# Kernel tuning notes

Measured on AMD Instinct MI355X. Metric: run time of the kernel, lower is better.

## Reference

```python
import jax, jax.numpy as jnp
import numpy as np

N, E, D, H = 50000, 800000, 128, 4
EPS = 1e-5


def setup_inputs() -> dict:
    key = jax.random.key(0)
    ks = jax.random.split(key, 12)
    s_in = 1.0 / np.sqrt(D)
    s_att = 1.0 / np.sqrt(D)
    inp = {
        "x": jax.random.normal(ks[0], (N, D), dtype=jnp.float32),
        "edge_index": jax.random.randint(ks[1], (2, E), 0, N, dtype=jnp.int32),
        # conv1 params: W [D, H*D], att_src/att_dst [H, D], bias [D]
        "W1": jax.random.normal(ks[2], (D, H * D), dtype=jnp.float32) * s_in,
        "as1": jax.random.normal(ks[3], (H, D), dtype=jnp.float32) * s_att,
        "ad1": jax.random.normal(ks[4], (H, D), dtype=jnp.float32) * s_att,
        "b1": jnp.zeros((D,), dtype=jnp.float32),
        "g1": jnp.ones((D,), dtype=jnp.float32),
        "be1": jnp.zeros((D,), dtype=jnp.float32),
        # conv2 params
        "W2": jax.random.normal(ks[5], (D, H * D), dtype=jnp.float32) * s_in,
        "as2": jax.random.normal(ks[6], (H, D), dtype=jnp.float32) * s_att,
        "ad2": jax.random.normal(ks[7], (H, D), dtype=jnp.float32) * s_att,
        "b2": jnp.zeros((D,), dtype=jnp.float32),
        "g2": jnp.ones((D,), dtype=jnp.float32),
        "be2": jnp.zeros((D,), dtype=jnp.float32),
    }
    return inp


def _gat_conv(x, src, dst, W, att_src, att_dst, bias):
    # project: [N, H, C]
    h = (x @ W).reshape(N, H, D)
    a_src = jnp.einsum("nhc,hc->nh", h, att_src)  # [N, H]
    a_dst = jnp.einsum("nhc,hc->nh", h, att_dst)  # [N, H]
    # attention logits per edge, softmax over incoming edges of each dst
    logits = jax.nn.leaky_relu(a_src[src] + a_dst[dst], negative_slope=0.2)  # [Etot, H]
    lmax = jax.ops.segment_max(logits, dst, num_segments=N)  # [N, H]
    p = jnp.exp(logits - lmax[dst])
    denom = jax.ops.segment_sum(p, dst, num_segments=N)  # [N, H]
    alpha = p / denom[dst]  # self-loops guarantee denom > 0
    # weighted scatter-add aggregation
    msg = h[src] * alpha[:, :, None]  # [Etot, H, C]
    out = jax.ops.segment_sum(msg, dst, num_segments=N)  # [N, H, C]
    return out.mean(axis=1) + bias  # concat=False: mean over heads


def _batchnorm_relu(x, gamma, beta):
    mu = x.mean(axis=0)
    var = x.var(axis=0)  # biased, as torch uses for normalization
    xn = (x - mu) * jax.lax.rsqrt(var + EPS)
    return jax.nn.relu(xn * gamma + beta)


def reference(x, edge_index, W1, as1, ad1, b1, g1, be1, W2, as2, ad2, b2, g2, be2):
    # add self loops (GATConv default add_self_loops=True)
    loop = jnp.arange(N, dtype=edge_index.dtype)
    src = jnp.concatenate([edge_index[0], loop])
    dst = jnp.concatenate([edge_index[1], loop])
    x = _batchnorm_relu(_gat_conv(x, src, dst, W1, as1, ad1, b1), g1, be1)
    x = _batchnorm_relu(_gat_conv(x, src, dst, W2, as2, ad2, b2), g2, be2)
    return x
```

## Files before the change

### kernel.cpp

```cpp
#include <hip/hip_runtime.h>
#include <hip/hip_bf16.h>
#include <hip/hip_fp16.h>
#include <math.h>

#define NN 50000
#define NP 50048
#define NE 800000
#define ET (NE + NN)
#define DF 128
#define NH 4
#define HD 512
#define BN_EPS 1e-5f

typedef __hip_bfloat16 bf16;
typedef __attribute__((ext_vector_type(8))) short bf16x8;
typedef __attribute__((ext_vector_type(4))) float f32x4;

__global__ __launch_bounds__(256) void cvt_x_bf16(const float* __restrict__ in, bf16* __restrict__ out) {
    int i = blockIdx.x * 256 + threadIdx.x;
    if (i >= NN * DF / 4) return;
    float4 v = reinterpret_cast<const float4*>(in)[i];
    union { bf16 b[4]; short4 s; } u;
    u.b[0] = __float2bfloat16(v.x); u.b[1] = __float2bfloat16(v.y);
    u.b[2] = __float2bfloat16(v.z); u.b[3] = __float2bfloat16(v.w);
    reinterpret_cast<short4*>(out)[i] = u.s;
}

__global__ __launch_bounds__(256) void make_wsd(const float* __restrict__ W1, const float* __restrict__ as1,
                                                const float* __restrict__ ad1,
                                                const float* __restrict__ W2, const float* __restrict__ as2,
                                                const float* __restrict__ ad2,
                                                float* __restrict__ wsd) {
    int t = blockIdx.x * 256 + threadIdx.x;
    if (t >= 2048) return;
    int layer = t >> 10;
    int o = (t >> 7) & 7;
    int d = t & 127;
    int h = o & 3;
    const float* W  = layer ? W2 : W1;
    const float* av = layer ? (o < 4 ? as2 : ad2) : (o < 4 ? as1 : ad1);
    const float* wrow = W + d * HD + h * DF;
    const float* arow = av + h * DF;
    float sum = 0.f;
    for (int c = 0; c < DF; ++c) sum += wrow[c] * arow[c];
    wsd[layer * 1024 + o * DF + d] = sum;
}

__global__ __launch_bounds__(256) void cvt_bt2(const float* __restrict__ W1, const float* __restrict__ W2,
                                               bf16* __restrict__ B1, bf16* __restrict__ B2) {
    int i = blockIdx.x * 256 + threadIdx.x;
    if (i >= 2 * DF * HD) return;
    int layer = i >> 16;
    int ii = i & 65535;
    int c = ii >> 9, k = ii & 511;
    int h = k >> 7, d = k & 127;
    const float* W = layer ? W2 : W1;
    bf16* B = layer ? B2 : B1;
    B[ii] = __float2bfloat16(0.25f * W[d * HD + h * DF + c]);
}

__global__ __launch_bounds__(256) void xscore(const bf16* __restrict__ X,
                                              const float* __restrict__ wsd,
                                              float* __restrict__ a_src,
                                              float* __restrict__ a_dst) {
    __shared__ float w[8][DF];
    reinterpret_cast<float4*>(&w[0][0])[threadIdx.x] = reinterpret_cast<const float4*>(wsd)[threadIdx.x];
    __syncthreads();
    const int n = blockIdx.x * 4 + (threadIdx.x >> 6);
    const int l = threadIdx.x & 63;
    unsigned xv = reinterpret_cast<const unsigned*>(X)[n * 64 + l];
    float x0 = __uint_as_float(xv << 16);
    float x1 = __uint_as_float(xv & 0xffff0000u);
    float v[8];
    #pragma unroll
    for (int o = 0; o < 8; ++o)
        v[o] = x0 * w[o][2 * l] + x1 * w[o][2 * l + 1];
    #pragma unroll
    for (int off = 1; off < 64; off <<= 1) {
        #pragma unroll
        for (int o = 0; o < 8; ++o) v[o] += __shfl_xor(v[o], off);
    }
    if (l == 0) {
        reinterpret_cast<float4*>(a_src)[n] = make_float4(v[0], v[1], v[2], v[3]);
        reinterpret_cast<float4*>(a_dst)[n] = make_float4(v[4], v[5], v[6], v[7]);
    }
}

__global__ __launch_bounds__(256) void count_rank(const int* __restrict__ ei, int* __restrict__ counts,
                                                  int* __restrict__ rank) {
    int e = (blockIdx.x * 256 + threadIdx.x) * 2;
    if (e >= ET) return;
    int d0, d1;
    if (e + 1 < NE) {
        int2 dd = *reinterpret_cast<const int2*>(ei + NE + e);
        d0 = dd.x; d1 = dd.y;
    } else {
        d0 = (e < NE) ? ei[NE + e] : (e - NE);
        d1 = (e + 1 < NE) ? ei[NE + e + 1] : (e + 1 - NE);
    }
    rank[e]     = atomicAdd(&counts[d0 << 4], 1);
    rank[e + 1] = atomicAdd(&counts[d1 << 4], 1);
}

__global__ __launch_bounds__(256) void scan1(const int* __restrict__ counts, int* __restrict__ bsum) {
    __shared__ int sd[256];
    int i = blockIdx.x * 256 + threadIdx.x;
    sd[threadIdx.x] = (i < NN) ? counts[i << 4] : 0;
    __syncthreads();
    for (int s = 128; s > 0; s >>= 1) {
        if (threadIdx.x < s) sd[threadIdx.x] += sd[threadIdx.x + s];
        __syncthreads();
    }
    if (threadIdx.x == 0) bsum[blockIdx.x] = sd[0];
}

__global__ __launch_bounds__(256) void scan2(int* __restrict__ bsum, int nb) {
    __shared__ int sd[256];
    int i = threadIdx.x;
    int v = (i < nb) ? bsum[i] : 0;
    sd[i] = v;
    __syncthreads();
    for (int s = 1; s < 256; s <<= 1) {
        int t = sd[i];
        int u = (i >= s) ? sd[i - s] : 0;
        __syncthreads();
        sd[i] = t + u;
        __syncthreads();
    }
    if (i < nb) bsum[i] = sd[i] - v;
}

__global__ __launch_bounds__(256) void scan3(const int* __restrict__ counts, const int* __restrict__ bsum,
                                             int* __restrict__ row_ptr) {
    __shared__ int sd[256];
    int i = blockIdx.x * 256 + threadIdx.x;
    int v = (i < NN) ? counts[i << 4] : 0;
    sd[threadIdx.x] = v;
    __syncthreads();
    for (int s = 1; s < 256; s <<= 1) {
        int t = sd[threadIdx.x];
        int u = (threadIdx.x >= s) ? sd[threadIdx.x - s] : 0;
        __syncthreads();
        sd[threadIdx.x] = t + u;
        __syncthreads();
    }
    int excl = sd[threadIdx.x] - v + bsum[blockIdx.x];
    if (i < NN) row_ptr[i] = excl;
    if (i == 0) row_ptr[NN] = ET;
}

__global__ __launch_bounds__(256) void fill_scatter(const int* __restrict__ ei, const int* __restrict__ rank,
                                                    const int* __restrict__ row_ptr, int* __restrict__ col) {
    int e = (blockIdx.x * 256 + threadIdx.x) * 2;
    if (e >= ET) return;
    int s0, d0, s1, d1;
    if (e + 1 < NE) {
        int2 ss = *reinterpret_cast<const int2*>(ei + e);
        int2 dd = *reinterpret_cast<const int2*>(ei + NE + e);
        s0 = ss.x; s1 = ss.y; d0 = dd.x; d1 = dd.y;
    } else {
        if (e < NE) { s0 = ei[e]; d0 = ei[NE + e]; } else { s0 = d0 = e - NE; }
        if (e + 1 < NE) { s1 = ei[e + 1]; d1 = ei[NE + e + 1]; } else { s1 = d1 = e + 1 - NE; }
    }
    int2 rk = *reinterpret_cast<const int2*>(rank + e);
    col[row_ptr[d0] + rk.x] = s0;
    col[row_ptr[d1] + rk.y] = s1;
}

__global__ __launch_bounds__(256) void edge_alpha(const float* __restrict__ a_src,
                                                  const float* __restrict__ a_dst,
                                                  const int* __restrict__ row_ptr,
                                                  const int* __restrict__ col,
                                                  uint4* __restrict__ rec) {
    const int n = blockIdx.x * 4 + (threadIdx.x >> 6);
    const int l = threadIdx.x & 63;
    const int start = row_ptr[n], end = row_ptr[n + 1];
    const float4 ad4 = reinterpret_cast<const float4*>(a_dst)[n];
    const float4* __restrict__ as4 = reinterpret_cast<const float4*>(a_src);
    if (end - start <= 64) {
        const int j = start + l;
        int cj = 0;
        float lv[4] = {-1e30f, -1e30f, -1e30f, -1e30f};
        if (j < end) {
            cj = col[j];
            float4 a = as4[cj];
            lv[0] = a.x + ad4.x; lv[1] = a.y + ad4.y; lv[2] = a.z + ad4.z; lv[3] = a.w + ad4.w;
            #pragma unroll
            for (int h = 0; h < 4; ++h) lv[h] = lv[h] > 0.f ? lv[h] : 0.2f * lv[h];
        }
        float m[4], p[4], s[4];
        #pragma unroll
        for (int h = 0; h < 4; ++h) m[h] = lv[h];
        #pragma unroll
        for (int off = 1; off < 64; off <<= 1) {
            #pragma unroll
            for (int h = 0; h < 4; ++h) m[h] = fmaxf(m[h], __shfl_xor(m[h], off));
        }
        #pragma unroll
        for (int h = 0; h < 4; ++h) { p[h] = (j < end) ? __expf(lv[h] - m[h]) : 0.f; s[h] = p[h]; }
        #pragma unroll
        for (int off = 1; off < 64; off <<= 1) {
            #pragma unroll
            for (int h = 0; h < 4; ++h) s[h] += __shfl_xor(s[h], off);
        }
        if (j < end) {
            __half2 a01 = __floats2half2_rn(p[0] / s[0], p[1] / s[1]);
            __half2 a23 = __floats2half2_rn(p[2] / s[2], p[3] / s[3]);
            uint4 r;
            r.x = *reinterpret_cast<unsigned*>(&a01);
            r.y = *reinterpret_cast<unsigned*>(&a23);
            r.z = (unsigned)cj;
            r.w = 0;
            rec[j] = r;
        }
    } else {
        float m[4] = {-1e30f, -1e30f, -1e30f, -1e30f}, s[4] = {0.f, 0.f, 0.f, 0.f};
        for (int base = start; base < end; base += 64) {
            const int j = base + l;
            float lv[4] = {-1e30f, -1e30f, -1e30f, -1e30f};
            if (j < end) {
                float4 a = as4[col[j]];
                lv[0] = a.x + ad4.x; lv[1] = a.y + ad4.y; lv[2] = a.z + ad4.z; lv[3] = a.w + ad4.w;
                #pragma unroll
                for (int h = 0; h < 4; ++h) lv[h] = lv[h] > 0.f ? lv[h] : 0.2f * lv[h];
            }
            float cm[4], cp[4];
            #pragma unroll
            for (int h = 0; h < 4; ++h) cm[h] = lv[h];
            #pragma unroll
            for (int off = 1; off < 64; off <<= 1) {
                #pragma unroll
                for (int h = 0; h < 4; ++h) cm[h] = fmaxf(cm[h], __shfl_xor(cm[h], off));
            }
            #pragma unroll
            for (int h = 0; h < 4; ++h) {
                float nm = fmaxf(m[h], cm[h]);
                cp[h] = (j < end) ? __expf(lv[h] - nm) : 0.f;
                s[h] *= __expf(m[h] - nm);
                m[h] = nm;
            }
            #pragma unroll
            for (int off = 1; off < 64; off <<= 1) {
                #pragma unroll
                for (int h = 0; h < 4; ++h) cp[h] += __shfl_xor(cp[h], off);
            }
            #pragma unroll
            for (int h = 0; h < 4; ++h) s[h] += cp[h];
        }
        for (int base = start; base < end; base += 64) {
            const int j = base + l;
            if (j < end) {
                int cj = col[j];
                float4 a = as4[cj];
                float v0 = a.x + ad4.x, v1 = a.y + ad4.y, v2 = a.z + ad4.z, v3 = a.w + ad4.w;
                v0 = v0 > 0.f ? v0 : 0.2f * v0; v1 = v1 > 0.f ? v1 : 0.2f * v1;
                v2 = v2 > 0.f ? v2 : 0.2f * v2; v3 = v3 > 0.f ? v3 : 0.2f * v3;
                __half2 a01 = __floats2half2_rn(__expf(v0 - m[0]) / s[0], __expf(v1 - m[1]) / s[1]);
                __half2 a23 = __floats2half2_rn(__expf(v2 - m[2]) / s[2], __expf(v3 - m[3]) / s[3]);
                uint4 r;
                r.x = *reinterpret_cast<unsigned*>(&a01);
                r.y = *reinterpret_cast<unsigned*>(&a23);
                r.z = (unsigned)cj;
                r.w = 0;
                rec[j] = r;
            }
        }
    }
}

#define EDGE(xu, r) {                                                                \
    float lo = __uint_as_float((xu) << 16);                                          \
    float hi = __uint_as_float((xu) & 0xffff0000u);                                  \
    float2 f01 = __half22float2(*reinterpret_cast<const __half2*>(&(r).x));          \
    float2 f23 = __half22float2(*reinterpret_cast<const __half2*>(&(r).y));          \
    acc[0][0] += f01.x * lo; acc[0][1] += f01.x * hi;                                \
    acc[1][0] += f01.y * lo; acc[1][1] += f01.y * hi;                                \
    acc[2][0] += f23.x * lo; acc[2][1] += f23.x * hi;                                \
    acc[3][0] += f23.y * lo; acc[3][1] += f23.y * hi; }

__global__ __launch_bounds__(256) void aggregate_x(const bf16* __restrict__ X,
                                                   const uint4* __restrict__ rec,
                                                   const int* __restrict__ row_ptr,
                                                   bf16* __restrict__ aggX) {
    const int n = blockIdx.x * 4 + (threadIdx.x >> 6);
    const int l = threadIdx.x & 63;
    const int start = row_ptr[n], end = row_ptr[n + 1];
    const unsigned* __restrict__ X4 = reinterpret_cast<const unsigned*>(X);
    float acc[4][2] = {};
    int j = start;
    for (; j + 4 <= end; j += 4) {
        uint4 r0 = rec[j], r1 = rec[j + 1], r2 = rec[j + 2], r3 = rec[j + 3];
        unsigned x0 = X4[(size_t)r0.z * 64 + l];
        unsigned x1 = X4[(size_t)r1.z * 64 + l];
        unsigned x2 = X4[(size_t)r2.z * 64 + l];
        unsigned x3 = X4[(size_t)r3.z * 64 + l];
        EDGE(x0, r0) EDGE(x1, r1) EDGE(x2, r2) EDGE(x3, r3)
    }
    for (; j < end; ++j) {
        uint4 r0 = rec[j];
        unsigned x0 = X4[(size_t)r0.z * 64 + l];
        EDGE(x0, r0)
    }
    unsigned* outp = reinterpret_cast<unsigned*>(aggX) + (size_t)n * 256;
    #pragma unroll
    for (int h = 0; h < 4; ++h) {
        union { bf16 b; unsigned short u; } plo, phi;
        plo.b = __float2bfloat16(acc[h][0]);
        phi.b = __float2bfloat16(acc[h][1]);
        outp[h * 64 + l] = (unsigned)plo.u | ((unsigned)phi.u << 16);
    }
}

__global__ __launch_bounds__(256) void gemm_out(const bf16* __restrict__ A,
                                                const bf16* __restrict__ Bt,
                                                const float* __restrict__ bias,
                                                bf16* __restrict__ outb,
                                                float* __restrict__ stats, int M) {
    __shared__ __align__(16) char Bs[65536];
    __shared__ float ssum[128], ssq[128];
    const int tid = threadIdx.x;
    if (tid < 128) { ssum[tid] = 0.f; ssq[tid] = 0.f; }
    const int m0 = blockIdx.x * 64;
    const char* Ab = (const char*)A + (size_t)m0 * 1024;
    const char* Bb = (const char*)Bt;
    auto stageB = [&](int ph) {
        #pragma unroll
        for (int i = 0; i < 16; ++i) {
            int d = (tid + i * 256) * 16;
            int c = d >> 9;
            int kb = d & 511;
            int src = c * 1024 + ph * 512 + (kb ^ ((c & 7) << 4));
            __builtin_amdgcn_global_load_lds(
                (const __attribute__((address_space(1))) void*)(Bb + src),
                (__attribute__((address_space(3))) void*)(Bs + d), 16, 0, 0);
        }
    };
    const int lane = tid & 63;
    const int wave = tid >> 6;
    const int wm = (wave & 1) * 32;
    const int wnb = (wave >> 1) * 64;
    const int lr = lane & 15;
    const int lkb = (lane >> 4) * 16;
    f32x4 acc[2][4] = {};
    const char* arow0 = Ab + (size_t)(wm + lr) * 1024 + lkb;
    const char* arow1 = Ab + (size_t)(wm + 16 + lr) * 1024 + lkb;
    stageB(0);
    #pragma unroll
    for (int ph = 0; ph < 2; ++ph) {
        __syncthreads();
        #pragma unroll 4
        for (int kk = 0; kk < 8; ++kk) {
            int kg = ph * 512 + kk * 64;
            bf16x8 a0 = *(const bf16x8*)(arow0 + kg);
            bf16x8 a1 = *(const bf16x8*)(arow1 + kg);
            int kb = kk * 64 + lkb;
            #pragma unroll
            for (int nf = 0; nf < 4; ++nf) {
                int c = wnb + nf * 16 + lr;
                bf16x8 b = *(const bf16x8*)(Bs + c * 512 + (kb ^ ((c & 7) << 4)));
                acc[0][nf] = __builtin_amdgcn_mfma_f32_16x16x32_bf16(a0, b, acc[0][nf], 0, 0, 0);
                acc[1][nf] = __builtin_amdgcn_mfma_f32_16x16x32_bf16(a1, b, acc[1][nf], 0, 0, 0);
            }
        }
        if (ph == 0) {
            __syncthreads();
            stageB(1);
        }
    }
    const int orow = (lane >> 4) * 4;
    float bcol[4];
    #pragma unroll
    for (int nf = 0; nf < 4; ++nf) bcol[nf] = bias[wnb + nf * 16 + lr];
    #pragma unroll
    for (int nf = 0; nf < 4; ++nf) {
        float cs = 0.f, cq = 0.f;
        int c = wnb + nf * 16 + lr;
        #pragma unroll
        for (int mi = 0; mi < 2; ++mi) {
            #pragma unroll
            for (int r = 0; r < 4; ++r) {
                int gr = m0 + wm + mi * 16 + orow + r;
                if (gr < M) {
                    float v = acc[mi][nf][r] + bcol[nf];
                    outb[(size_t)gr * DF + c] = __float2bfloat16(v);
                    cs += v; cq += v * v;
                }
            }
        }
        atomicAdd(&ssum[c], cs);
        atomicAdd(&ssq[c], cq);
    }
    __syncthreads();
    if (tid < 128) {
        atomicAdd(&stats[tid], ssum[tid]);
        atomicAdd(&stats[128 + tid], ssq[tid]);
    }
}

__device__ __forceinline__ void bn_core(const uint4 v, int c0, const float* stats,
                                        const float* gamma, const float* beta, float* o) {
    float xv[8];
    xv[0] = __uint_as_float(v.x << 16); xv[1] = __uint_as_float(v.x & 0xffff0000u);
    xv[2] = __uint_as_float(v.y << 16); xv[3] = __uint_as_float(v.y & 0xffff0000u);
    xv[4] = __uint_as_float(v.z << 16); xv[5] = __uint_as_float(v.z & 0xffff0000u);
    xv[6] = __uint_as_float(v.w << 16); xv[7] = __uint_as_float(v.w & 0xffff0000u);
    #pragma unroll
    for (int k = 0; k < 8; ++k) {
        int c = c0 + k;
        float mu = stats[c] * (1.f / NN);
        float var = stats[128 + c] * (1.f / NN) - mu * mu;
        o[k] = fmaxf((xv[k] - mu) * rsqrtf(var + BN_EPS) * gamma[c] + beta[c], 0.f);
    }
}

__global__ __launch_bounds__(256) void bn_apply_bf16(const bf16* __restrict__ x, const float* __restrict__ stats,
                                                     const float* __restrict__ gamma, const float* __restrict__ beta,
                                                     bf16* __restrict__ out) {
    int i = blockIdx.x * 256 + threadIdx.x;
    if (i >= NN * DF / 8) return;
    uint4 v = reinterpret_cast<const uint4*>(x)[i];
    float o[8];
    bn_core(v, (i * 8) & 127, stats, gamma, beta, o);
    uint4 w;
    unsigned short* wb = reinterpret_cast<unsigned short*>(&w);
    #pragma unroll
    for (int k = 0; k < 8; ++k) {
        union { bf16 b; unsigned short u; } t;
        t.b = __float2bfloat16(o[k]);
        wb[k] = t.u;
    }
    reinterpret_cast<uint4*>(out)[i] = w;
}

__global__ __launch_bounds__(256) void bn_apply_f32(const bf16* __restrict__ x, const float* __restrict__ stats,
                                                    const float* __restrict__ gamma, const float* __restrict__ beta,
                                                    float* __restrict__ out) {
    int i = blockIdx.x * 256 + threadIdx.x;
    if (i >= NN * DF / 8) return;
    uint4 v = reinterpret_cast<const uint4*>(x)[i];
    float o[8];
    bn_core(v, (i * 8) & 127, stats, gamma, beta, o);
    float4* op = reinterpret_cast<float4*>(out) + (size_t)i * 2;
    op[0] = make_float4(o[0], o[1], o[2], o[3]);
    op[1] = make_float4(o[4], o[5], o[6], o[7]);
}

extern "C" void kernel_launch(void* const* d_in, const int* in_sizes, int n_in,
                              void* d_out, int out_size, void* d_ws, size_t ws_size,
                              hipStream_t stream) {
    (void)in_sizes; (void)n_in; (void)out_size; (void)ws_size;
    const float* x   = (const float*)d_in[0];
    const int*   ei  = (const int*)d_in[1];
    const float* W1  = (const float*)d_in[2];
    const float* as1 = (const float*)d_in[3];
    const float* ad1 = (const float*)d_in[4];
    const float* b1  = (const float*)d_in[5];
    const float* g1  = (const float*)d_in[6];
    const float* be1 = (const float*)d_in[7];
    const float* W2  = (const float*)d_in[8];
    const float* as2 = (const float*)d_in[9];
    const float* ad2 = (const float*)d_in[10];
    const float* b2  = (const float*)d_in[11];
    const float* g2  = (const float*)d_in[12];
    const float* be2 = (const float*)d_in[13];
    float* out = (float*)d_out;

    char* ws = (char*)d_ws;
    size_t off = 0;
    auto alloc = [&](size_t bytes) -> void* {
        void* p = ws + off;
        off += (bytes + 255) & ~(size_t)255;
        return p;
    };
    bf16*   aggX    = (bf16*)alloc((size_t)NP * HD * 2);
    bf16*   xb      = (bf16*)alloc((size_t)NP * DF * 2);
    bf16*   Bt2a    = (bf16*)alloc((size_t)DF * HD * 2);
    bf16*   Bt2b    = (bf16*)alloc((size_t)DF * HD * 2);
    float*  wsd     = (float*)alloc(2 * 1024 * 4);
    float*  a_src   = (float*)alloc((size_t)NN * NH * 4);
    float*  a_dst   = (float*)alloc((size_t)NN * NH * 4);
    int*    row_ptr = (int*)alloc((size_t)(NN + 1) * 4);
    int*    bsum    = (int*)alloc(256 * 4);
    int*    colidx  = (int*)alloc((size_t)ET * 4);
    uint4*  rec     = (uint4*)alloc((size_t)ET * 16);
    bf16*   agg     = (bf16*)alloc((size_t)NN * DF * 2);
    float*  stats   = (float*)alloc(256 * 4);
    int*    counts  = (int*)agg;
    int*    rank    = (int*)((char*)agg + ((size_t)NP << 6));

    const int NB = (NN + 255) / 256;
    const int EB2 = (ET / 2 + 255) / 256;
    const int BNB = (NN * DF / 8 + 255) / 256;

    cvt_x_bf16<<<(NN * DF / 4 + 255) / 256, 256, 0, stream>>>(x, xb);
    make_wsd<<<8, 256, 0, stream>>>(W1, as1, ad1, W2, as2, ad2, wsd);
    cvt_bt2<<<(2 * DF * HD + 255) / 256, 256, 0, stream>>>(W1, W2, Bt2a, Bt2b);
    hipMemsetAsync(counts, 0, (size_t)NP << 6, stream);
    count_rank<<<EB2, 256, 0, stream>>>(ei, counts, rank);
    scan1<<<NB, 256, 0, stream>>>(counts, bsum);
    scan2<<<1, 256, 0, stream>>>(bsum, NB);
    scan3<<<NB, 256, 0, stream>>>(counts, bsum, row_ptr);
    fill_scatter<<<EB2, 256, 0, stream>>>(ei, rank, row_ptr, colidx);

    xscore<<<NN / 4, 256, 0, stream>>>(xb, wsd, a_src, a_dst);
    edge_alpha<<<NN / 4, 256, 0, stream>>>(a_src, a_dst, row_ptr, colidx, rec);
    aggregate_x<<<NN / 4, 256, 0, stream>>>(xb, rec, row_ptr, aggX);
    hipMemsetAsync(stats, 0, 256 * 4, stream);
    gemm_out<<<NP / 64, 256, 0, stream>>>(aggX, Bt2a, b1, agg, stats, NN);
    bn_apply_bf16<<<BNB, 256, 0, stream>>>(agg, stats, g1, be1, xb);

    xscore<<<NN / 4, 256, 0, stream>>>(xb, wsd + 1024, a_src, a_dst);
    edge_alpha<<<NN / 4, 256, 0, stream>>>(a_src, a_dst, row_ptr, colidx, rec);
    aggregate_x<<<NN / 4, 256, 0, stream>>>(xb, rec, row_ptr, aggX);
    hipMemsetAsync(stats, 0, 256 * 4, stream);
    gemm_out<<<NP / 64, 256, 0, stream>>>(aggX, Bt2b, b2, agg, stats, NN);
    bn_apply_f32<<<BNB, 256, 0, stream>>>(agg, stats, g2, be2, out);
}
```

Baseline: 388.4 us.

## Fuse edge softmax with neighbor aggregation and fold stats reset into xscore

Merges the edge_alpha and aggregate_x kernels into one agg_fused kernel. For nodes with degree at most 64, the per-edge attention record now lives in LDS instead of global memory. High-degree nodes still write records to global memory and read them back after a block fence. The stats memset is replaced by zeroing inside xscore, which removes one launch per layer. The goal is to cut kernel launches and the global round trip of the per-edge records. The fused kernel may need more registers, and the low-degree loop reads LDS records past deg in groups of 4, which are padded with zero alpha.

```diff
diff --git a/kernel.cpp b/kernel.cpp
--- a/kernel.cpp
+++ b/kernel.cpp
@@ -62,7 +62,10 @@
 __global__ __launch_bounds__(256) void xscore(const bf16* __restrict__ X,
                                               const float* __restrict__ wsd,
                                               float* __restrict__ a_src,
-                                              float* __restrict__ a_dst) {
+                                              float* __restrict__ a_dst,
+                                              float* __restrict__ stats) {
+    if (blockIdx.x == 0 && threadIdx.x < 64)
+        reinterpret_cast<float4*>(stats)[threadIdx.x] = make_float4(0.f, 0.f, 0.f, 0.f);
     __shared__ float w[8][DF];
     reinterpret_cast<float4*>(&w[0][0])[threadIdx.x] = reinterpret_cast<const float4*>(wsd)[threadIdx.x];
     __syncthreads();
@@ -167,17 +170,34 @@
     col[row_ptr[d1] + rk.y] = s1;
 }
 
-__global__ __launch_bounds__(256) void edge_alpha(const float* __restrict__ a_src,
-                                                  const float* __restrict__ a_dst,
-                                                  const int* __restrict__ row_ptr,
-                                                  const int* __restrict__ col,
-                                                  uint4* __restrict__ rec) {
-    const int n = blockIdx.x * 4 + (threadIdx.x >> 6);
+#define EDGE(xu, r) {                                                                \
+    float lo = __uint_as_float((xu) << 16);                                          \
+    float hi = __uint_as_float((xu) & 0xffff0000u);                                  \
+    float2 f01 = __half22float2(*reinterpret_cast<const __half2*>(&(r).x));          \
+    float2 f23 = __half22float2(*reinterpret_cast<const __half2*>(&(r).y));          \
+    acc[0][0] += f01.x * lo; acc[0][1] += f01.x * hi;                                \
+    acc[1][0] += f01.y * lo; acc[1][1] += f01.y * hi;                                \
+    acc[2][0] += f23.x * lo; acc[2][1] += f23.x * hi;                                \
+    acc[3][0] += f23.y * lo; acc[3][1] += f23.y * hi; }
+
+__global__ __launch_bounds__(256) void agg_fused(const bf16* __restrict__ X,
+                                                 const float* __restrict__ a_src,
+                                                 const float* __restrict__ a_dst,
+                                                 const int* __restrict__ row_ptr,
+                                                 const int* __restrict__ col,
+                                                 uint4* __restrict__ rec,
+                                                 bf16* __restrict__ aggX) {
+    __shared__ __align__(16) uint4 lrec[4][64];
+    const int w = threadIdx.x >> 6;
+    const int n = blockIdx.x * 4 + w;
     const int l = threadIdx.x & 63;
     const int start = row_ptr[n], end = row_ptr[n + 1];
+    const int deg = end - start;
     const float4 ad4 = reinterpret_cast<const float4*>(a_dst)[n];
     const float4* __restrict__ as4 = reinterpret_cast<const float4*>(a_src);
-    if (end - start <= 64) {
+    const unsigned* __restrict__ X4 = reinterpret_cast<const unsigned*>(X);
+    float acc[4][2] = {};
+    if (deg <= 64) {
         const int j = start + l;
         int cj = 0;
         float lv[4] = {-1e30f, -1e30f, -1e30f, -1e30f};
@@ -203,15 +223,22 @@
             #pragma unroll
             for (int h = 0; h < 4; ++h) s[h] += __shfl_xor(s[h], off);
         }
-        if (j < end) {
-            __half2 a01 = __floats2half2_rn(p[0] / s[0], p[1] / s[1]);
-            __half2 a23 = __floats2half2_rn(p[2] / s[2], p[3] / s[3]);
-            uint4 r;
-            r.x = *reinterpret_cast<unsigned*>(&a01);
-            r.y = *reinterpret_cast<unsigned*>(&a23);
-            r.z = (unsigned)cj;
-            r.w = 0;
-            rec[j] = r;
+        __half2 a01 = __floats2half2_rn(p[0] / s[0], p[1] / s[1]);
+        __half2 a23 = __floats2half2_rn(p[2] / s[2], p[3] / s[3]);
+        uint4 r;
+        r.x = *reinterpret_cast<unsigned*>(&a01);
+        r.y = *reinterpret_cast<unsigned*>(&a23);
+        r.z = (unsigned)cj;
+        r.w = 0;
+        lrec[w][l] = r;
+        __builtin_amdgcn_wave_barrier();
+        for (int i = 0; i < deg; i += 4) {
+            uint4 r0 = lrec[w][i], r1 = lrec[w][i + 1], r2 = lrec[w][i + 2], r3 = lrec[w][i + 3];
+            unsigned x0 = X4[(size_t)r0.z * 64 + l];
+            unsigned x1 = X4[(size_t)r1.z * 64 + l];
+            unsigned x2 = X4[(size_t)r2.z * 64 + l];
+            unsigned x3 = X4[(size_t)r3.z * 64 + l];
+            EDGE(x0, r0) EDGE(x1, r1) EDGE(x2, r2) EDGE(x3, r3)
         }
     } else {
         float m[4] = {-1e30f, -1e30f, -1e30f, -1e30f}, s[4] = {0.f, 0.f, 0.f, 0.f};
@@ -265,41 +292,21 @@
                 rec[j] = r;
             }
         }
-    }
-}
-
-#define EDGE(xu, r) {                                                                \
-    float lo = __uint_as_float((xu) << 16);                                          \
-    float hi = __uint_as_float((xu) & 0xffff0000u);                                  \
-    float2 f01 = __half22float2(*reinterpret_cast<const __half2*>(&(r).x));          \
-    float2 f23 = __half22float2(*reinterpret_cast<const __half2*>(&(r).y));          \
-    acc[0][0] += f01.x * lo; acc[0][1] += f01.x * hi;                                \
-    acc[1][0] += f01.y * lo; acc[1][1] += f01.y * hi;                                \
-    acc[2][0] += f23.x * lo; acc[2][1] += f23.x * hi;                                \
-    acc[3][0] += f23.y * lo; acc[3][1] += f23.y * hi; }
-
-__global__ __launch_bounds__(256) void aggregate_x(const bf16* __restrict__ X,
-                                                   const uint4* __restrict__ rec,
-                                                   const int* __restrict__ row_ptr,
-                                                   bf16* __restrict__ aggX) {
-    const int n = blockIdx.x * 4 + (threadIdx.x >> 6);
-    const int l = threadIdx.x & 63;
-    const int start = row_ptr[n], end = row_ptr[n + 1];
-    const unsigned* __restrict__ X4 = reinterpret_cast<const unsigned*>(X);
-    float acc[4][2] = {};
-    int j = start;
-    for (; j + 4 <= end; j += 4) {
-        uint4 r0 = rec[j], r1 = rec[j + 1], r2 = rec[j + 2], r3 = rec[j + 3];
-        unsigned x0 = X4[(size_t)r0.z * 64 + l];
-        unsigned x1 = X4[(size_t)r1.z * 64 + l];
-        unsigned x2 = X4[(size_t)r2.z * 64 + l];
-        unsigned x3 = X4[(size_t)r3.z * 64 + l];
-        EDGE(x0, r0) EDGE(x1, r1) EDGE(x2, r2) EDGE(x3, r3)
-    }
-    for (; j < end; ++j) {
-        uint4 r0 = rec[j];
-        unsigned x0 = X4[(size_t)r0.z * 64 + l];
-        EDGE(x0, r0)
+        __threadfence_block();
+        int j = start;
+        for (; j + 4 <= end; j += 4) {
+            uint4 r0 = rec[j], r1 = rec[j + 1], r2 = rec[j + 2], r3 = rec[j + 3];
+            unsigned x0 = X4[(size_t)r0.z * 64 + l];
+            unsigned x1 = X4[(size_t)r1.z * 64 + l];
+            unsigned x2 = X4[(size_t)r2.z * 64 + l];
+            unsigned x3 = X4[(size_t)r3.z * 64 + l];
+            EDGE(x0, r0) EDGE(x1, r1) EDGE(x2, r2) EDGE(x3, r3)
+        }
+        for (; j < end; ++j) {
+            uint4 r0 = rec[j];
+            unsigned x0 = X4[(size_t)r0.z * 64 + l];
+            EDGE(x0, r0)
+        }
     }
     unsigned* outp = reinterpret_cast<unsigned*>(aggX) + (size_t)n * 256;
     #pragma unroll
@@ -502,17 +509,13 @@
     scan3<<<NB, 256, 0, stream>>>(counts, bsum, row_ptr);
     fill_scatter<<<EB2, 256, 0, stream>>>(ei, rank, row_ptr, colidx);
 
-    xscore<<<NN / 4, 256, 0, stream>>>(xb, wsd, a_src, a_dst);
-    edge_alpha<<<NN / 4, 256, 0, stream>>>(a_src, a_dst, row_ptr, colidx, rec);
-    aggregate_x<<<NN / 4, 256, 0, stream>>>(xb, rec, row_ptr, aggX);
-    hipMemsetAsync(stats, 0, 256 * 4, stream);
+    xscore<<<NN / 4, 256, 0, stream>>>(xb, wsd, a_src, a_dst, stats);
+    agg_fused<<<NN / 4, 256, 0, stream>>>(xb, a_src, a_dst, row_ptr, colidx, rec, aggX);
     gemm_out<<<NP / 64, 256, 0, stream>>>(aggX, Bt2a, b1, agg, stats, NN);
     bn_apply_bf16<<<BNB, 256, 0, stream>>>(agg, stats, g1, be1, xb);
 
-    xscore<<<NN / 4, 256, 0, stream>>>(xb, wsd + 1024, a_src, a_dst);
-    edge_alpha<<<NN / 4, 256, 0, stream>>>(a_src, a_dst, row_ptr, colidx, rec);
-    aggregate_x<<<NN / 4, 256, 0, stream>>>(xb, rec, row_ptr, aggX);
-    hipMemsetAsync(stats, 0, 256 * 4, stream);
+    xscore<<<NN / 4, 256, 0, stream>>>(xb, wsd + 1024, a_src, a_dst, stats);
+    agg_fused<<<NN / 4, 256, 0, stream>>>(xb, a_src, a_dst, row_ptr, colidx, rec, aggX);
     gemm_out<<<NP / 64, 256, 0, stream>>>(aggX, Bt2b, b2, agg, stats, NN);
     bn_apply_f32<<<BNB, 256, 0, stream>>>(agg, stats, g2, be2, out);
 }
```

Measured after the change: 336.7 us. -13.3%, faster.
